# Kernel tuning notes

Measured on AMD Instinct MI355X. Metric: run time of the kernel, lower is better.

The kernel has to match this reference:

```python
import jax, jax.numpy as jnp
import numpy as np

L, H, D, BINS = 4, 8, 512, 16
HD = D // H
DFF = 4 * D
EPS = 1e-5


def _ln(x, g, b):
    mu = jnp.mean(x, axis=-1, keepdims=True)
    var = jnp.var(x, axis=-1, keepdims=True)
    return (x - mu) * jax.lax.rsqrt(var + EPS) * g + b


def setup_inputs() -> dict:
    key = jax.random.key(0)
    ks = jax.random.split(key, 24)
    B, N, F = 8, 1024, 4
    s = 0.02
    inp = {
        'slot_features': jax.random.normal(ks[0], (B, N, F), jnp.float32),
        'distance_matrix': jax.random.uniform(ks[1], (B, N, N), jnp.float32),
        'slot_mask': jnp.ones((B, N), dtype=bool),
        # input projection (Linear 4->D, then ReLU, then LayerNorm)
        'in_w': jax.random.normal(ks[2], (F, D), jnp.float32) * s,
        'in_b': jnp.zeros((D,), jnp.float32),
        'in_g': jnp.ones((D,), jnp.float32),
        'in_beta': jnp.zeros((D,), jnp.float32),
        # learnable distance bias, init linspace(0,-2) per head
        'dist_bias': jnp.tile(jnp.linspace(0.0, -2.0, BINS, dtype=jnp.float32)[None, :], (H, 1)),
        # per-layer stacked params (weights stored [in,out])
        'qkv_w': jax.random.normal(ks[3], (L, D, 3 * D), jnp.float32) * s,
        'qkv_b': jnp.zeros((L, 3 * D), jnp.float32),
        'out_w': jax.random.normal(ks[4], (L, D, D), jnp.float32) * s,
        'out_b': jnp.zeros((L, D), jnp.float32),
        'ffn_w1': jax.random.normal(ks[5], (L, D, DFF), jnp.float32) * s,
        'ffn_b1': jnp.zeros((L, DFF), jnp.float32),
        'ffn_w2': jax.random.normal(ks[6], (L, DFF, D), jnp.float32) * s,
        'ffn_b2': jnp.zeros((L, D), jnp.float32),
        'n1_g': jnp.ones((L, D), jnp.float32),
        'n1_b': jnp.zeros((L, D), jnp.float32),
        'n2_g': jnp.ones((L, D), jnp.float32),
        'n2_b': jnp.zeros((L, D), jnp.float32),
        'op_w': jax.random.normal(ks[7], (D, D), jnp.float32) * s,
        'op_b': jnp.zeros((D,), jnp.float32),
    }
    return inp


def _distance_bias(distance_matrix, slot_mask, dist_bias):
    # (B,H,N,N) additive attention bias from binned normalized distances
    max_dist = jnp.clip(jnp.max(distance_matrix, axis=(-1, -2), keepdims=True), 1e-6, None)
    norm_dist = distance_matrix / max_dist
    bin_idx = jnp.clip((norm_dist * (BINS - 1)).astype(jnp.int32), 0, BINS - 1)  # (B,N,N)
    bias = jnp.transpose(dist_bias.T[bin_idx], (0, 3, 1, 2))  # (B,N,N,H)->(B,H,N,N)
    pad = ~(slot_mask[:, :, None] & slot_mask[:, None, :])  # (B,N,N)
    return jnp.where(pad[:, None, :, :], -jnp.inf, bias)


def reference(slot_features, distance_matrix, slot_mask, in_w, in_b, in_g, in_beta,
              dist_bias, qkv_w, qkv_b, out_w, out_b, ffn_w1, ffn_b1, ffn_w2, ffn_b2,
              n1_g, n1_b, n2_g, n2_b, op_w, op_b):
    B, N, _ = slot_features.shape
    h = _ln(jax.nn.relu(slot_features @ in_w + in_b), in_g, in_beta)  # (B,N,D)
    attn_bias = _distance_bias(distance_matrix, slot_mask, dist_bias)  # (B,H,N,N)
    scale = 1.0 / jnp.sqrt(jnp.float32(HD))
    for i in range(L):
        hn = _ln(h, n1_g[i], n1_b[i])
        qkv = (hn @ qkv_w[i] + qkv_b[i]).reshape(B, N, 3, H, HD)
        q, k, v = (jnp.transpose(qkv[:, :, j], (0, 2, 1, 3)) for j in range(3))  # (B,H,N,HD)
        scores = jnp.einsum('bhnd,bhmd->bhnm', q, k) * scale + attn_bias
        attn = jax.nn.softmax(scores, axis=-1)
        o = jnp.einsum('bhnm,bhmd->bhnd', attn, v)
        o = jnp.transpose(o, (0, 2, 1, 3)).reshape(B, N, D)
        h = h + (o @ out_w[i] + out_b[i])
        hn2 = _ln(h, n2_g[i], n2_b[i])
        ff = jax.nn.gelu(hn2 @ ffn_w1[i] + ffn_b1[i], approximate=False) @ ffn_w2[i] + ffn_b2[i]
        h = h + ff
    return h @ op_w + op_b
```

## Files before the change

### kernel.cpp

```cpp
#include <hip/hip_runtime.h>


typedef __attribute__((ext_vector_type(8))) short short8;
typedef __attribute__((ext_vector_type(4))) float f32x4;

__device__ __forceinline__ float b2f(unsigned short u){
  return __uint_as_float(((unsigned)u) << 16);
}
__device__ __forceinline__ unsigned short f2b(float f){
  unsigned u = __float_as_uint(f);
  u += 0x7fffU + ((u >> 16) & 1U);
  return (unsigned short)(u >> 16);
}
__device__ __forceinline__ void gload16(const void* g, void* l){
  __builtin_amdgcn_global_load_lds((const __attribute__((address_space(1))) void*)g,
                                   (__attribute__((address_space(3))) void*)l, 16, 0, 0);
}

__global__ void transpose_w(const float* __restrict__ src, unsigned short* __restrict__ dst,
                            int K, int N){
  __shared__ float tile[32][33];
  const float* s = src + (size_t)blockIdx.z * K * N;
  unsigned short* d = dst + (size_t)blockIdx.z * K * N;
  int j = threadIdx.x & 31, i0 = threadIdx.x >> 5;
  int kt = blockIdx.y * 32, nt = blockIdx.x * 32;
#pragma unroll
  for (int s4 = 0; s4 < 4; ++s4){
    int i = i0 + s4 * 8;
    tile[i][j] = s[(size_t)(kt + i) * N + nt + j];
  }
  __syncthreads();
#pragma unroll
  for (int s4 = 0; s4 < 4; ++s4){
    int i = i0 + s4 * 8;
    d[(size_t)(nt + i) * K + kt + j] = f2b(tile[j][i]);
  }
}

__global__ void vt_kernel(const unsigned short* __restrict__ qkv, unsigned short* __restrict__ vt){
  __shared__ unsigned short tile[32][33];
  int tt = blockIdx.x, dt = blockIdx.y, bh = blockIdx.z;
  int b = bh >> 3, h = bh & 7;
  int j = threadIdx.x & 31, i0 = threadIdx.x >> 5;
#pragma unroll
  for (int s4 = 0; s4 < 4; ++s4){
    int i = i0 + s4 * 8;
    tile[i][j] = qkv[(size_t)(b * 1024 + tt * 32 + i) * 1536 + 1024 + h * 64 + dt * 32 + j];
  }
  __syncthreads();
#pragma unroll
  for (int s4 = 0; s4 < 4; ++s4){
    int i = i0 + s4 * 8;
    vt[(size_t)(bh * 64 + dt * 32 + i) * 1024 + tt * 32 + j] = tile[j][i];
  }
}

__global__ void bmax_kernel(const float* __restrict__ dist, unsigned* __restrict__ bmax){
  int b = blockIdx.x >> 5, sl = blockIdx.x & 31;
  const float* p = dist + (size_t)b * 1048576 + sl * 32768;
  int t = threadIdx.x;
  float m = 0.f;
  for (int i = t * 4; i < 32768; i += 1024){
    float4 v = *(const float4*)(p + i);
    m = fmaxf(m, fmaxf(fmaxf(v.x, v.y), fmaxf(v.z, v.w)));
  }
#pragma unroll
  for (int o = 1; o < 64; o <<= 1) m = fmaxf(m, __shfl_xor(m, o));
  __shared__ float wm[4];
  if ((t & 63) == 0) wm[t >> 6] = m;
  __syncthreads();
  if (t == 0){
    m = fmaxf(fmaxf(wm[0], wm[1]), fmaxf(wm[2], wm[3]));
    atomicMax(bmax + b, __float_as_uint(m));
  }
}

__global__ void bins_kernel(const float* __restrict__ dist, const unsigned* __restrict__ bmax,
                            unsigned char* __restrict__ out){
  int idx = (blockIdx.x * 256 + threadIdx.x) * 4;
  int b = idx >> 20;
  float mx = fmaxf(__uint_as_float(bmax[b]), 1e-6f);
  float4 v = *(const float4*)(dist + idx);
  int b0 = (int)((v.x / mx) * 15.0f); b0 = b0 < 0 ? 0 : (b0 > 15 ? 15 : b0);
  int b1 = (int)((v.y / mx) * 15.0f); b1 = b1 < 0 ? 0 : (b1 > 15 ? 15 : b1);
  int b2 = (int)((v.z / mx) * 15.0f); b2 = b2 < 0 ? 0 : (b2 > 15 ? 15 : b2);
  int b3 = (int)((v.w / mx) * 15.0f); b3 = b3 < 0 ? 0 : (b3 > 15 ? 15 : b3);
  uchar4 o; o.x = (unsigned char)b0; o.y = (unsigned char)b1; o.z = (unsigned char)b2; o.w = (unsigned char)b3;
  *(uchar4*)(out + idx) = o;
}

__global__ void inproj_kernel(const float* __restrict__ x, const float* __restrict__ w,
                              const float* __restrict__ b, const float* __restrict__ g,
                              const float* __restrict__ be, float* __restrict__ h){
  int t = threadIdx.x, wv = t >> 6, lane = t & 63;
  int row = blockIdx.x * 4 + wv;
  float x0 = x[row * 4 + 0], x1 = x[row * 4 + 1], x2 = x[row * 4 + 2], x3 = x[row * 4 + 3];
  int c0 = lane * 4, c1 = 256 + lane * 4;
  float4 v0, v1; float s = 0.f, sq = 0.f;
  {
    float4 w0 = *(const float4*)(w + c0), w1 = *(const float4*)(w + 512 + c0);
    float4 w2 = *(const float4*)(w + 1024 + c0), w3 = *(const float4*)(w + 1536 + c0);
    float4 bb = *(const float4*)(b + c0);
    v0.x = fmaxf(0.f, x0*w0.x + x1*w1.x + x2*w2.x + x3*w3.x + bb.x);
    v0.y = fmaxf(0.f, x0*w0.y + x1*w1.y + x2*w2.y + x3*w3.y + bb.y);
    v0.z = fmaxf(0.f, x0*w0.z + x1*w1.z + x2*w2.z + x3*w3.z + bb.z);
    v0.w = fmaxf(0.f, x0*w0.w + x1*w1.w + x2*w2.w + x3*w3.w + bb.w);
    s += v0.x + v0.y + v0.z + v0.w;
    sq += v0.x*v0.x + v0.y*v0.y + v0.z*v0.z + v0.w*v0.w;
  }
  {
    float4 w0 = *(const float4*)(w + c1), w1 = *(const float4*)(w + 512 + c1);
    float4 w2 = *(const float4*)(w + 1024 + c1), w3 = *(const float4*)(w + 1536 + c1);
    float4 bb = *(const float4*)(b + c1);
    v1.x = fmaxf(0.f, x0*w0.x + x1*w1.x + x2*w2.x + x3*w3.x + bb.x);
    v1.y = fmaxf(0.f, x0*w0.y + x1*w1.y + x2*w2.y + x3*w3.y + bb.y);
    v1.z = fmaxf(0.f, x0*w0.z + x1*w1.z + x2*w2.z + x3*w3.z + bb.z);
    v1.w = fmaxf(0.f, x0*w0.w + x1*w1.w + x2*w2.w + x3*w3.w + bb.w);
    s += v1.x + v1.y + v1.z + v1.w;
    sq += v1.x*v1.x + v1.y*v1.y + v1.z*v1.z + v1.w*v1.w;
  }
#pragma unroll
  for (int o = 1; o < 64; o <<= 1){ s += __shfl_xor(s, o); sq += __shfl_xor(sq, o); }
  float mu = s * (1.f / 512.f);
  float var = sq * (1.f / 512.f) - mu * mu;
  float rs = rsqrtf(var + 1e-5f);
  float* hp = h + (size_t)row * 512;
  {
    float4 gg = *(const float4*)(g + c0), bb = *(const float4*)(be + c0);
    float4 o4;
    o4.x = (v0.x - mu) * rs * gg.x + bb.x; o4.y = (v0.y - mu) * rs * gg.y + bb.y;
    o4.z = (v0.z - mu) * rs * gg.z + bb.z; o4.w = (v0.w - mu) * rs * gg.w + bb.w;
    *(float4*)(hp + c0) = o4;
  }
  {
    float4 gg = *(const float4*)(g + c1), bb = *(const float4*)(be + c1);
    float4 o4;
    o4.x = (v1.x - mu) * rs * gg.x + bb.x; o4.y = (v1.y - mu) * rs * gg.y + bb.y;
    o4.z = (v1.z - mu) * rs * gg.z + bb.z; o4.w = (v1.w - mu) * rs * gg.w + bb.w;
    *(float4*)(hp + c1) = o4;
  }
}

__global__ void ln_kernel(const float* __restrict__ h, const float* __restrict__ g,
                          const float* __restrict__ b, unsigned short* __restrict__ out){
  int t = threadIdx.x, wv = t >> 6, lane = t & 63;
  int row = blockIdx.x * 4 + wv;
  const float* hp = h + (size_t)row * 512;
  int c0 = lane * 4, c1 = 256 + lane * 4;
  float4 u0 = *(const float4*)(hp + c0);
  float4 u1 = *(const float4*)(hp + c1);
  float s = u0.x + u0.y + u0.z + u0.w + u1.x + u1.y + u1.z + u1.w;
  float sq = u0.x*u0.x + u0.y*u0.y + u0.z*u0.z + u0.w*u0.w
           + u1.x*u1.x + u1.y*u1.y + u1.z*u1.z + u1.w*u1.w;
#pragma unroll
  for (int o = 1; o < 64; o <<= 1){ s += __shfl_xor(s, o); sq += __shfl_xor(sq, o); }
  float mu = s * (1.f / 512.f);
  float var = sq * (1.f / 512.f) - mu * mu;
  float rs = rsqrtf(var + 1e-5f);
  unsigned short* op = out + (size_t)row * 512;
  {
    float4 gg = *(const float4*)(g + c0), bb = *(const float4*)(b + c0);
    ushort4 o4;
    o4.x = f2b((u0.x - mu) * rs * gg.x + bb.x); o4.y = f2b((u0.y - mu) * rs * gg.y + bb.y);
    o4.z = f2b((u0.z - mu) * rs * gg.z + bb.z); o4.w = f2b((u0.w - mu) * rs * gg.w + bb.w);
    *(ushort4*)(op + c0) = o4;
  }
  {
    float4 gg = *(const float4*)(g + c1), bb = *(const float4*)(b + c1);
    ushort4 o4;
    o4.x = f2b((u1.x - mu) * rs * gg.x + bb.x); o4.y = f2b((u1.y - mu) * rs * gg.y + bb.y);
    o4.z = f2b((u1.z - mu) * rs * gg.z + bb.z); o4.w = f2b((u1.w - mu) * rs * gg.w + bb.w);
    *(ushort4*)(op + c1) = o4;
  }
}

#define EPI_BF 0
#define EPI_RESID 1
#define EPI_GELU 2
#define EPI_RESID_BF 3
#define EPI_F32 4

template<int N, int K, int EPI>
__global__ __launch_bounds__(256) void gemm_k(
    const unsigned short* __restrict__ A,
    const unsigned short* __restrict__ Bt,
    const float* __restrict__ bias,
    float* __restrict__ resid,
    unsigned short* __restrict__ outb,
    float* __restrict__ outf)
{
  __shared__ unsigned short As[4096], Bs[4096];
  int t = threadIdx.x, w = t >> 6, lane = t & 63;
  int l15 = lane & 15, g = lane >> 4;
  int bm = blockIdx.x, bn = blockIdx.y;
  int wm = w >> 1, wn = w & 1;
  f32x4 acc[4][4];
#pragma unroll
  for (int i = 0; i < 4; ++i)
#pragma unroll
    for (int j = 0; j < 4; ++j) acc[i][j] = (f32x4){0.f, 0.f, 0.f, 0.f};

  for (int kt = 0; kt < K / 32; ++kt){
#pragma unroll
    for (int it = 0; it < 2; ++it){
      int ci = it * 4 + w;
      int o = ci * 1024 + lane * 16;
      int row = o >> 6, sp = (o >> 4) & 3;
      int sl = sp ^ ((row >> 1) & 3);
      gload16(A + (size_t)(bm * 128 + row) * K + kt * 32 + sl * 8, As + ci * 512);
      gload16(Bt + (size_t)(bn * 128 + row) * K + kt * 32 + sl * 8, Bs + ci * 512);
    }
    __syncthreads();
    short8 af[4], bf[4];
#pragma unroll
    for (int i = 0; i < 4; ++i){
      int row = wm * 64 + i * 16 + l15;
      int sp = g ^ ((row >> 1) & 3);
      af[i] = *(const short8*)(As + row * 32 + sp * 8);
    }
#pragma unroll
    for (int j = 0; j < 4; ++j){
      int row = wn * 64 + j * 16 + l15;
      int sp = g ^ ((row >> 1) & 3);
      bf[j] = *(const short8*)(Bs + row * 32 + sp * 8);
    }
#pragma unroll
    for (int i = 0; i < 4; ++i)
#pragma unroll
      for (int j = 0; j < 4; ++j)
        acc[i][j] = __builtin_amdgcn_mfma_f32_16x16x32_bf16(af[i], bf[j], acc[i][j], 0, 0, 0);
    __syncthreads();
  }
  int rbase = bm * 128 + wm * 64, cbase = bn * 128 + wn * 64;
#pragma unroll
  for (int j = 0; j < 4; ++j){
    int col = cbase + j * 16 + l15;
    float bs = bias[col];
#pragma unroll
    for (int i = 0; i < 4; ++i){
#pragma unroll
      for (int r = 0; r < 4; ++r){
        int row = rbase + i * 16 + g * 4 + r;
        size_t idx = (size_t)row * N + col;
        float x = acc[i][j][r] + bs;
        if constexpr (EPI == EPI_BF){
          outb[idx] = f2b(x);
        } else if constexpr (EPI == EPI_RESID){
          resid[idx] = resid[idx] + x;
        } else if constexpr (EPI == EPI_GELU){
          float y = 0.5f * x * (1.f + erff(x * 0.70710678118654752f));
          outb[idx] = f2b(y);
        } else if constexpr (EPI == EPI_RESID_BF){
          float y = resid[idx] + x;
          resid[idx] = y;
          outb[idx] = f2b(y);
        } else {
          outf[idx] = x;
        }
      }
    }
  }
}

__global__ __launch_bounds__(256) void attn_kernel(
    const unsigned short* __restrict__ qkv,
    const unsigned short* __restrict__ vt,
    const unsigned char* __restrict__ bins,
    const float* __restrict__ dist_bias,
    unsigned short* __restrict__ o_out)
{
  __shared__ unsigned short Ks[64 * 64];
  __shared__ unsigned short Vs[64 * 64];
  __shared__ unsigned short Ps[4][16 * 64];
  int bhx = blockIdx.x, qt = blockIdx.y;
  int b = bhx & 7, h = bhx >> 3;
  int bh = b * 8 + h;
  int t = threadIdx.x, w = t >> 6, lane = t & 63;
  int l15 = lane & 15, g = lane >> 4, rx = lane & 7;
  unsigned short* Psw = Ps[w];
  float lutv = dist_bias[h * 16 + l15];

  int qrow_frag = qt * 64 + w * 16 + l15;
  const unsigned short* qp = qkv + ((size_t)(b * 1024 + qrow_frag)) * 1536 + h * 64;
  short8 qf[2];
#pragma unroll
  for (int c = 0; c < 2; ++c){
    short8 raw = *(const short8*)(qp + c * 32 + g * 8);
#pragma unroll
    for (int e = 0; e < 8; ++e)
      raw[e] = (short)f2b(b2f((unsigned short)raw[e]) * 0.125f);
    qf[c] = raw;
  }

  float m_run[4], l_run[4];
  f32x4 acc_o[4];
#pragma unroll
  for (int r = 0; r < 4; ++r){ m_run[r] = -1e30f; l_run[r] = 0.f; }
#pragma unroll
  for (int d = 0; d < 4; ++d) acc_o[d] = (f32x4){0.f, 0.f, 0.f, 0.f};

  int qrow_c = qt * 64 + w * 16 + g * 4;
  int srow_lo = lane >> 3;
  int sslot = lane & 7;

  for (int kt = 0; kt < 16; ++kt){
    __syncthreads();
#pragma unroll
    for (int it = 0; it < 2; ++it){
      int ci = it * 4 + w;
      int row = ci * 8 + srow_lo;
      int sl = sslot ^ (row & 7);
      gload16(qkv + (size_t)(b * 1024 + kt * 64 + row) * 1536 + 512 + h * 64 + sl * 8,
              Ks + ci * 512);
      gload16(vt + (size_t)(bh * 64 + row) * 1024 + kt * 64 + sl * 8,
              Vs + ci * 512);
    }
    __syncthreads();

    f32x4 sv[4];
#pragma unroll
    for (int ks = 0; ks < 4; ++ks){
      f32x4 a = (f32x4){0.f, 0.f, 0.f, 0.f};
#pragma unroll
      for (int c = 0; c < 2; ++c){
        short8 kf = *(const short8*)(Ks + (ks * 16 + l15) * 64 + ((c * 4 + g) ^ rx) * 8);
        a = __builtin_amdgcn_mfma_f32_16x16x32_bf16(qf[c], kf, a, 0, 0, 0);
      }
      sv[ks] = a;
    }
    unsigned bw[4];
#pragma unroll
    for (int r = 0; r < 4; ++r)
      bw[r] = *(const unsigned*)(bins + (size_t)(b * 1024 + qrow_c + r) * 1024 + kt * 64 + l15 * 4);
#pragma unroll
    for (int r = 0; r < 4; ++r)
#pragma unroll
      for (int ks = 0; ks < 4; ++ks){
        unsigned word = __shfl(bw[r], g * 16 + ks * 4 + (l15 >> 2));
        int bin = (word >> ((l15 & 3) * 8)) & 255;
        sv[ks][r] += __shfl(lutv, bin);
      }
    float mt[4];
#pragma unroll
    for (int r = 0; r < 4; ++r)
      mt[r] = fmaxf(fmaxf(sv[0][r], sv[1][r]), fmaxf(sv[2][r], sv[3][r]));
#pragma unroll
    for (int o = 1; o < 16; o <<= 1)
#pragma unroll
      for (int r = 0; r < 4; ++r) mt[r] = fmaxf(mt[r], __shfl_xor(mt[r], o));
    float mnew[4], alpha[4];
#pragma unroll
    for (int r = 0; r < 4; ++r){
      mnew[r] = fmaxf(m_run[r], mt[r]);
      alpha[r] = __expf(m_run[r] - mnew[r]);
      m_run[r] = mnew[r];
    }
    float rs_[4] = {0.f, 0.f, 0.f, 0.f};
#pragma unroll
    for (int ks = 0; ks < 4; ++ks)
#pragma unroll
      for (int r = 0; r < 4; ++r){
        float p = __expf(sv[ks][r] - mnew[r]);
        rs_[r] += p;
        int prow = g * 4 + r;
        Psw[prow * 64 + ((ks * 2 + (l15 >> 3)) ^ (prow & 7)) * 8 + (l15 & 7)] = f2b(p);
      }
#pragma unroll
    for (int o = 1; o < 16; o <<= 1)
#pragma unroll
      for (int r = 0; r < 4; ++r) rs_[r] += __shfl_xor(rs_[r], o);
#pragma unroll
    for (int r = 0; r < 4; ++r) l_run[r] = l_run[r] * alpha[r] + rs_[r];
#pragma unroll
    for (int d = 0; d < 4; ++d){
      f32x4 ao = acc_o[d];
#pragma unroll
      for (int r = 0; r < 4; ++r) ao[r] *= alpha[r];
      acc_o[d] = ao;
    }
#pragma unroll
    for (int c = 0; c < 2; ++c){
      short8 pa = *(const short8*)(Psw + l15 * 64 + ((c * 4 + g) ^ rx) * 8);
#pragma unroll
      for (int d = 0; d < 4; ++d){
        short8 vf = *(const short8*)(Vs + (d * 16 + l15) * 64 + ((c * 4 + g) ^ rx) * 8);
        acc_o[d] = __builtin_amdgcn_mfma_f32_16x16x32_bf16(pa, vf, acc_o[d], 0, 0, 0);
      }
    }
  }
#pragma unroll
  for (int d = 0; d < 4; ++d)
#pragma unroll
    for (int r = 0; r < 4; ++r){
      float v = acc_o[d][r] / l_run[r];
      size_t row = (size_t)(b * 1024 + qrow_c + r);
      o_out[row * 512 + h * 64 + d * 16 + l15] = f2b(v);
    }
}

extern "C" void kernel_launch(void* const* d_in, const int* in_sizes, int n_in,
                              void* d_out, int out_size, void* d_ws, size_t ws_size,
                              hipStream_t stream) {
  const float* x     = (const float*)d_in[0];
  const float* dist  = (const float*)d_in[1];
  const float* in_w  = (const float*)d_in[3];
  const float* in_b  = (const float*)d_in[4];
  const float* in_g  = (const float*)d_in[5];
  const float* in_be = (const float*)d_in[6];
  const float* dbias = (const float*)d_in[7];
  const float* qkv_w = (const float*)d_in[8];
  const float* qkv_b = (const float*)d_in[9];
  const float* out_w = (const float*)d_in[10];
  const float* out_b = (const float*)d_in[11];
  const float* f1_w  = (const float*)d_in[12];
  const float* f1_b  = (const float*)d_in[13];
  const float* f2_w  = (const float*)d_in[14];
  const float* f2_b  = (const float*)d_in[15];
  const float* n1g   = (const float*)d_in[16];
  const float* n1b   = (const float*)d_in[17];
  const float* n2g   = (const float*)d_in[18];
  const float* n2b   = (const float*)d_in[19];
  const float* op_w  = (const float*)d_in[20];
  const float* op_b  = (const float*)d_in[21];

  char* ws = (char*)d_ws;
  size_t off = 0;
  auto alloc = [&](size_t bytes){ size_t o = off; off += (bytes + 255) & ~(size_t)255; return o; };
  unsigned short* wqkv  = (unsigned short*)(ws + alloc((size_t)4 * 1536 * 512 * 2));
  unsigned short* wout  = (unsigned short*)(ws + alloc((size_t)4 * 512 * 512 * 2));
  unsigned short* wf1   = (unsigned short*)(ws + alloc((size_t)4 * 2048 * 512 * 2));
  unsigned short* wf2   = (unsigned short*)(ws + alloc((size_t)4 * 512 * 2048 * 2));
  unsigned short* wop   = (unsigned short*)(ws + alloc((size_t)512 * 512 * 2));
  float*          h     = (float*)(ws + alloc((size_t)8192 * 512 * 4));
  unsigned short* actbf = (unsigned short*)(ws + alloc((size_t)8192 * 512 * 2));
  unsigned short* qkvff = (unsigned short*)(ws + alloc((size_t)8192 * 2048 * 2));
  unsigned char*  binsb = (unsigned char*)(ws + alloc((size_t)8 * 1024 * 1024));
  unsigned*       bmax  = (unsigned*)(ws + alloc(256));
  unsigned short* vt    = qkvff + (size_t)8192 * 1536;
  (void)ws_size; (void)in_sizes; (void)n_in; (void)out_size;

  hipMemsetAsync(bmax, 0, 32, stream);
  transpose_w<<<dim3(48, 16, 4), 256, 0, stream>>>(qkv_w, wqkv, 512, 1536);
  transpose_w<<<dim3(16, 16, 4), 256, 0, stream>>>(out_w, wout, 512, 512);
  transpose_w<<<dim3(64, 16, 4), 256, 0, stream>>>(f1_w, wf1, 512, 2048);
  transpose_w<<<dim3(16, 64, 4), 256, 0, stream>>>(f2_w, wf2, 2048, 512);
  transpose_w<<<dim3(16, 16, 1), 256, 0, stream>>>(op_w, wop, 512, 512);
  bmax_kernel<<<256, 256, 0, stream>>>(dist, bmax);
  bins_kernel<<<8192, 256, 0, stream>>>(dist, bmax, binsb);
  inproj_kernel<<<2048, 256, 0, stream>>>(x, in_w, in_b, in_g, in_be, h);

  for (int l = 0; l < 4; ++l){
    ln_kernel<<<2048, 256, 0, stream>>>(h, n1g + l * 512, n1b + l * 512, actbf);
    gemm_k<1536, 512, EPI_BF><<<dim3(64, 12), 256, 0, stream>>>(
        actbf, wqkv + (size_t)l * 1536 * 512, qkv_b + l * 1536, nullptr, qkvff, nullptr);
    vt_kernel<<<dim3(32, 2, 64), 256, 0, stream>>>(qkvff, vt);
    attn_kernel<<<dim3(64, 16), 256, 0, stream>>>(qkvff, vt, binsb, dbias, actbf);
    gemm_k<512, 512, EPI_RESID><<<dim3(64, 4), 256, 0, stream>>>(
        actbf, wout + (size_t)l * 512 * 512, out_b + l * 512, h, nullptr, nullptr);
    ln_kernel<<<2048, 256, 0, stream>>>(h, n2g + l * 512, n2b + l * 512, actbf);
    gemm_k<2048, 512, EPI_GELU><<<dim3(64, 16), 256, 0, stream>>>(
        actbf, wf1 + (size_t)l * 2048 * 512, f1_b + l * 2048, nullptr, qkvff, nullptr);
    gemm_k<512, 2048, EPI_RESID_BF><<<dim3(64, 4), 256, 0, stream>>>(
        qkvff, wf2 + (size_t)l * 512 * 2048, f2_b + l * 512, h, actbf, nullptr);
  }
  gemm_k<512, 512, EPI_F32><<<dim3(64, 4), 256, 0, stream>>>(
      actbf, wop, op_b, nullptr, nullptr, (float*)d_out);
}
```

Measured before the change: 1.076 ms.

## Double-buffer attention K/V tiles and pre-permute distance bins to MFMA layout

The attention kernel now keeps two LDS buffers for K and V, so the next key tile is loaded asynchronously while the current one is computed, leaving one barrier per iteration instead of two. The bins kernel writes bin bytes in a permuted order that matches the MFMA accumulator layout, so each lane reads its four bins directly and the per-element shuffle in the attention loop goes away. The cost is double the K/V shared memory, which may lower occupancy, and a strided, less coalesced read pattern in the bins kernel.

```diff
diff --git a/kernel.cpp b/kernel.cpp
--- a/kernel.cpp
+++ b/kernel.cpp
@@ -77,16 +77,18 @@
 
 __global__ void bins_kernel(const float* __restrict__ dist, const unsigned* __restrict__ bmax,
                             unsigned char* __restrict__ out){
-  int idx = (blockIdx.x * 256 + threadIdx.x) * 4;
-  int b = idx >> 20;
+  int flat = blockIdx.x * 256 + threadIdx.x;
+  int l15 = flat & 15, kt = (flat >> 4) & 15, q = (flat >> 8) & 1023, b = flat >> 18;
   float mx = fmaxf(__uint_as_float(bmax[b]), 1e-6f);
-  float4 v = *(const float4*)(dist + idx);
-  int b0 = (int)((v.x / mx) * 15.0f); b0 = b0 < 0 ? 0 : (b0 > 15 ? 15 : b0);
-  int b1 = (int)((v.y / mx) * 15.0f); b1 = b1 < 0 ? 0 : (b1 > 15 ? 15 : b1);
-  int b2 = (int)((v.z / mx) * 15.0f); b2 = b2 < 0 ? 0 : (b2 > 15 ? 15 : b2);
-  int b3 = (int)((v.w / mx) * 15.0f); b3 = b3 < 0 ? 0 : (b3 > 15 ? 15 : b3);
-  uchar4 o; o.x = (unsigned char)b0; o.y = (unsigned char)b1; o.z = (unsigned char)b2; o.w = (unsigned char)b3;
-  *(uchar4*)(out + idx) = o;
+  const float* p = dist + ((size_t)(b * 1024 + q)) * 1024 + kt * 64 + l15;
+  unsigned wd = 0;
+#pragma unroll
+  for (int ks = 0; ks < 4; ++ks){
+    float v = p[ks * 16];
+    int bi = (int)((v / mx) * 15.0f); bi = bi < 0 ? 0 : (bi > 15 ? 15 : bi);
+    wd |= (unsigned)bi << (ks * 8);
+  }
+  *(unsigned*)(out + ((size_t)(b * 1024 + q)) * 1024 + kt * 64 + l15 * 4) = wd;
 }
 
 __global__ void inproj_kernel(const float* __restrict__ x, const float* __restrict__ w,
@@ -269,8 +271,8 @@
     const float* __restrict__ dist_bias,
     unsigned short* __restrict__ o_out)
 {
-  __shared__ unsigned short Ks[64 * 64];
-  __shared__ unsigned short Vs[64 * 64];
+  __shared__ unsigned short Ks[2][64 * 64];
+  __shared__ unsigned short Vs[2][64 * 64];
   __shared__ unsigned short Ps[4][16 * 64];
   int bhx = blockIdx.x, qt = blockIdx.y;
   int b = bhx & 7, h = bhx >> 3;
@@ -303,19 +305,28 @@
   int srow_lo = lane >> 3;
   int sslot = lane & 7;
 
-  for (int kt = 0; kt < 16; ++kt){
-    __syncthreads();
+  auto STAGE = [&](int buf, int kt){
 #pragma unroll
     for (int it = 0; it < 2; ++it){
       int ci = it * 4 + w;
       int row = ci * 8 + srow_lo;
       int sl = sslot ^ (row & 7);
       gload16(qkv + (size_t)(b * 1024 + kt * 64 + row) * 1536 + 512 + h * 64 + sl * 8,
-              Ks + ci * 512);
+              &Ks[buf][ci * 512]);
       gload16(vt + (size_t)(bh * 64 + row) * 1024 + kt * 64 + sl * 8,
-              Vs + ci * 512);
-    }
-    __syncthreads();
+              &Vs[buf][ci * 512]);
+    }
+  };
+
+  STAGE(0, 0);
+  __syncthreads();
+  int cur = 0;
+
+  for (int kt = 0; kt < 16; ++kt){
+    if (kt < 15) STAGE(cur ^ 1, kt + 1);
+
+    const unsigned short* Kc = Ks[cur];
+    const unsigned short* Vc = Vs[cur];
 
     f32x4 sv[4];
 #pragma unroll
@@ -323,7 +334,7 @@
       f32x4 a = (f32x4){0.f, 0.f, 0.f, 0.f};
 #pragma unroll
       for (int c = 0; c < 2; ++c){
-        short8 kf = *(const short8*)(Ks + (ks * 16 + l15) * 64 + ((c * 4 + g) ^ rx) * 8);
+        short8 kf = *(const short8*)(Kc + (ks * 16 + l15) * 64 + ((c * 4 + g) ^ rx) * 8);
         a = __builtin_amdgcn_mfma_f32_16x16x32_bf16(qf[c], kf, a, 0, 0, 0);
       }
       sv[ks] = a;
@@ -336,8 +347,7 @@
     for (int r = 0; r < 4; ++r)
 #pragma unroll
       for (int ks = 0; ks < 4; ++ks){
-        unsigned word = __shfl(bw[r], g * 16 + ks * 4 + (l15 >> 2));
-        int bin = (word >> ((l15 & 3) * 8)) & 255;
+        int bin = (bw[r] >> (ks * 8)) & 255;
         sv[ks][r] += __shfl(lutv, bin);
       }
     float mt[4];
@@ -383,10 +393,12 @@
       short8 pa = *(const short8*)(Psw + l15 * 64 + ((c * 4 + g) ^ rx) * 8);
 #pragma unroll
       for (int d = 0; d < 4; ++d){
-        short8 vf = *(const short8*)(Vs + (d * 16 + l15) * 64 + ((c * 4 + g) ^ rx) * 8);
+        short8 vf = *(const short8*)(Vc + (d * 16 + l15) * 64 + ((c * 4 + g) ^ rx) * 8);
         acc_o[d] = __builtin_amdgcn_mfma_f32_16x16x32_bf16(pa, vf, acc_o[d], 0, 0, 0);
       }
     }
+    __syncthreads();
+    cur ^= 1;
   }
 #pragma unroll
   for (int d = 0; d < 4; ++d)
```

Result: slower. 1.126 ms (+4.6%).
